# Performance work log

Hardware: AMD Instinct MI355X
Metric: run time of the kernel (lower is better)

The kernel has to match this reference:

```python
import jax, jax.numpy as jnp
import numpy as np

TEMP = 1.0
PRIOR = 0.2
THRESHOLD = 0.5
EPS = 1.1920929e-07  # torch float32 eps used by probs_to_logits / clamp_probs


def setup_inputs() -> dict:
    key = jax.random.key(0)
    k1, k2, k3, k4, k5 = jax.random.split(key, 5)
    B, L, D = 8, 8192, 256
    hidden = jax.random.normal(k1, (B, L, D), dtype=jnp.float32)
    # q/k projections are initialized to identity in the module; perturb slightly
    Wq = jnp.eye(D, dtype=jnp.float32) + 0.02 * jax.random.normal(k2, (D, D), dtype=jnp.float32)
    Wk = jnp.eye(D, dtype=jnp.float32) + 0.02 * jax.random.normal(k3, (D, D), dtype=jnp.float32)
    # uniform noise for the RelaxedBernoulli reparameterized sample
    noise = jax.random.uniform(k4, (B, L), dtype=jnp.float32)
    # ragged lengths -> contiguous attention mask (1s then 0s), as the module assumes
    lengths = jax.random.randint(k5, (B,), L // 2, L + 1)
    attention_mask = (jnp.arange(L)[None, :] < lengths[:, None]).astype(jnp.float32)
    return {"hidden": hidden, "Wq": Wq, "Wk": Wk, "noise": noise, "attention_mask": attention_mask}


def _binomial_loss(k, n, p):
    # -log Binomial(n, p).log_prob(k) / n
    logp = (jax.scipy.special.gammaln(n + 1.0)
            - jax.scipy.special.gammaln(k + 1.0)
            - jax.scipy.special.gammaln(n - k + 1.0)
            + k * jnp.log(p) + (n - k) * jnp.log1p(-p))
    return -logp / n


def reference(hidden, Wq, Wk, noise, attention_mask):
    B, L, D = hidden.shape
    # F.normalize along last dim (eps=1e-12), then linear projections (no bias)
    hn = hidden / jnp.maximum(jnp.linalg.norm(hidden, axis=-1, keepdims=True), 1e-12)
    q = jnp.einsum('bld,ed->ble', hn[:, :-1], Wq)
    k = jnp.einsum('bld,ed->ble', hn[:, 1:], Wk)
    cos_sim = jnp.sum(q * k, axis=-1)                      # [B, L-1]
    probs = jnp.clip((1.0 - cos_sim) * 0.5, 0.0, 1.0)
    probs = jnp.pad(probs, ((0, 0), (1, 0)), constant_values=1.0)  # boundary forced at t=0

    # RelaxedBernoulli(temp, probs).rsample() with externally supplied uniforms
    p = jnp.clip(probs, EPS, 1.0 - EPS)
    logits = jnp.log(p) - jnp.log1p(-p)
    u = jnp.clip(noise, EPS, 1.0 - EPS)
    soft = jax.nn.sigmoid((logits + jnp.log(u) - jnp.log1p(-u)) / TEMP)
    hard = (soft > THRESHOLD).astype(soft.dtype)
    hard = jax.lax.stop_gradient(hard - soft) + soft       # straight-through

    # mask out boundaries in padding; force a boundary at the last real token
    hard = hard * attention_mask
    pad_mask = attention_mask == 0
    first_pad = pad_mask & (jnp.cumsum(pad_mask.astype(jnp.int32), axis=1) == 1)
    last_real = jnp.roll(first_pad, shift=-1, axis=1).at[:, -1].set(False)
    hard = jnp.maximum(hard, last_real.astype(hard.dtype))

    # downsample: mean-pool tokens within each boundary-delimited segment.
    # boundary==1 starts a new segment; segment id = cumsum(hard) - 1.
    hard_bin = jax.lax.stop_gradient(hard) > 0.5
    seg = jnp.cumsum(hard_bin.astype(jnp.int32), axis=1) - 1
    seg = jnp.clip(seg, 0, L - 1)
    flat_seg = (seg + jnp.arange(B, dtype=jnp.int32)[:, None] * L).reshape(-1)  # [B*L]
    w = attention_mask.reshape(-1)                                              # pads excluded
    sums = jax.ops.segment_sum(hidden.reshape(-1, D) * w[:, None], flat_seg, num_segments=B * L)
    cnts = jax.ops.segment_sum(w, flat_seg, num_segments=B * L)
    pooled = (sums / (cnts + 1e-9)[:, None]).reshape(B, L, D)  # [B, S_max<=L, D], zero-padded

    n_b = jnp.sum(hard, axis=1)                  # boundaries per batch row
    num_boundaries = jnp.sum(n_b)
    total_positions = jnp.sum(attention_mask)
    # gathered mask values at kept positions are all 1 -> prefix-ones of length n_b
    shortened_attention_mask = (jnp.arange(L)[None, :]
                                < jax.lax.stop_gradient(n_b)[:, None]).astype(jnp.float32)
    loss = _binomial_loss(num_boundaries, total_positions, PRIOR)
    return pooled, loss, num_boundaries, total_positions, shortened_attention_mask
```

## Files before the change

### kernel.cpp

```cpp
#include <hip/hip_runtime.h>
#include <hip/hip_bf16.h>
#include <math.h>

#define L_SEQ 8192
#define B_BATCH 8
#define D_DIM 256
#define BL (B_BATCH * L_SEQ)
#define EPS_F 1.1920929e-07f

typedef __attribute__((ext_vector_type(8))) short short8;
typedef __attribute__((ext_vector_type(4))) float f32x4;
typedef __attribute__((ext_vector_type(4))) unsigned short u16x4;


__device__ inline unsigned short f2bf(float x) {
    __hip_bfloat16 b = __float2bfloat16(x);
    return *(unsigned short*)&b;
}
__device__ inline float bf2f(unsigned short u) {
    __hip_bfloat16 b = *(__hip_bfloat16*)&u;
    return __bfloat162float(b);
}

__global__ __launch_bounds__(256) void k_matMpack(
    const float* __restrict__ Wq, const float* __restrict__ Wk,
    unsigned short* __restrict__ Bpack) {
    __shared__ float Aq[64][33];
    __shared__ float Ak[64][17];
    const int f   = blockIdx.x;
    const int k8  = f >> 4, ct = f & 15;
    const int tid = threadIdx.x;
    const int n   = tid & 15;
    const int k   = tid >> 4;
    float a0 = 0.f, a1 = 0.f;
    for (int e0 = 0; e0 < 256; e0 += 64) {
        for (int i = tid; i < 64 * 32; i += 256) {
            const int e = i >> 5, d = i & 31;
            Aq[e][d] = Wq[(e0 + e) * 256 + k8 * 32 + d];
        }
        for (int i = tid; i < 64 * 16; i += 256) {
            const int e = i >> 4, d = i & 15;
            Ak[e][d] = Wk[(e0 + e) * 256 + ct * 16 + d];
        }
        __syncthreads();
#pragma unroll 8
        for (int e = 0; e < 64; ++e) {
            a0 += Aq[e][k] * Ak[e][n];
            a1 += Aq[e][k + 16] * Ak[e][n];
        }
        __syncthreads();
    }
    const int col = ct * 16 + n;
    const float M0 = a0 - ((k8 * 32 + k)      == col ? 1.0f : 0.0f);
    const float M1 = a1 - ((k8 * 32 + k + 16) == col ? 1.0f : 0.0f);
    const unsigned short h0 = f2bf(M0), h1 = f2bf(M1);
    const unsigned short l0 = f2bf(M0 - bf2f(h0)), l1 = f2bf(M1 - bf2f(h1));
    unsigned short* dstH = Bpack + (size_t)(k8 * 16 + ct) * 512;
    unsigned short* dstL = dstH + 128 * 512;
    const int q0 = k >> 3, j0 = k & 7;
    const int q1 = (k + 16) >> 3;
    dstH[(q0 * 16 + n) * 8 + j0] = h0;
    dstH[(q1 * 16 + n) * 8 + j0] = h1;
    dstL[(q0 * 16 + n) * 8 + j0] = l0;
    dstL[(q1 * 16 + n) * 8 + j0] = l1;
}

#define RS 264
#define MM(A,Bv,C) __builtin_amdgcn_mfma_f32_16x16x32_bf16((A),(Bv),(C),0,0,0)
#define MFMA8(V0,V1,BN) \
    acc[0][0]=MM(V0,BN##_0,acc[0][0]); acc[0][1]=MM(V0,BN##_1,acc[0][1]); \
    acc[0][2]=MM(V0,BN##_2,acc[0][2]); acc[0][3]=MM(V0,BN##_3,acc[0][3]); \
    acc[1][0]=MM(V1,BN##_0,acc[1][0]); acc[1][1]=MM(V1,BN##_1,acc[1][1]); \
    acc[1][2]=MM(V1,BN##_2,acc[1][2]); acc[1][3]=MM(V1,BN##_3,acc[1][3]);
#define LOADB(BN,S) \
    BN##_0 = Bld[(((S) * 16) + wc4 + 0) * 64]; \
    BN##_1 = Bld[(((S) * 16) + wc4 + 1) * 64]; \
    BN##_2 = Bld[(((S) * 16) + wc4 + 2) * 64]; \
    BN##_3 = Bld[(((S) * 16) + wc4 + 3) * 64];
#define STRIP_HL(S,BN) { \
    const int co = ((S) & 7) * 32; \
    const short8 hv0 = *(const short8*)(hA0 + co), hv1 = *(const short8*)(hA1 + co); \
    const short8 lv0 = *(const short8*)(lA0 + co), lv1 = *(const short8*)(lA1 + co); \
    MFMA8(hv0, hv1, BN); \
    MFMA8(lv0, lv1, BN); \
    LOADB(BN, (S) + 3); }
#define STRIP_H(S,BN) { \
    const int co = ((S) & 7) * 32; \
    const short8 hv0 = *(const short8*)(hA0 + co), hv1 = *(const short8*)(hA1 + co); \
    MFMA8(hv0, hv1, BN); \
    if ((S) + 3 < 16) { LOADB(BN, (S) + 3); } }

__global__ __launch_bounds__(256, 2) void k_cosmfma(
    const float* __restrict__ hidden, const unsigned short* __restrict__ Bpack,
    const float* __restrict__ noise, unsigned char* __restrict__ hard) {
    __shared__ __attribute__((aligned(16))) unsigned short hiA[33 * RS];
    __shared__ __attribute__((aligned(16))) unsigned short loA[33 * RS];
    __shared__ float Vpart[4][32];
    __shared__ float dots[32];

    const int tid  = threadIdx.x;
    const int lane = tid & 63;
    const int w    = tid >> 6;
    const int wc4  = w * 4;
    const int T0   = blockIdx.x * 32;

    const short8* __restrict__ Bld = (const short8*)Bpack + lane;

    short8 bA_0, bA_1, bA_2, bA_3, bB_0, bB_1, bB_2, bB_3, bC_0, bC_1, bC_2, bC_3;
    LOADB(bA, 0);
    LOADB(bB, 1);
    LOADB(bC, 2);

    {
        const int r0 = w * 8;
        int tokA = T0 - 1 + r0; if (tokA < 0) tokA = 0;
        float4 vb0 = ((const float4*)hidden)[(size_t)tokA * 64 + lane];
        float4 vb1 = ((const float4*)hidden)[(size_t)(T0 + r0) * 64 + lane];
        float4 hp4 = {0.f, 0.f, 0.f, 0.f};
#pragma unroll 1
        for (int ii = 0; ii <= 8; ++ii) {
            const float4 vcur = vb0;
            vb0 = vb1;
            if (ii + 2 <= 8)
                vb1 = ((const float4*)hidden)[(size_t)(T0 + r0 + ii + 1) * 64 + lane];
            float ss = vcur.x * vcur.x + vcur.y * vcur.y + vcur.z * vcur.z + vcur.w * vcur.w;
#pragma unroll
            for (int sh = 32; sh >= 1; sh >>= 1) ss += __shfl_xor(ss, sh);
            const float inv = 1.0f / fmaxf(sqrtf(ss), 1e-12f);
            float4 h4;
            h4.x = vcur.x * inv; h4.y = vcur.y * inv;
            h4.z = vcur.z * inv; h4.w = vcur.w * inv;
            const unsigned short hx = f2bf(h4.x), hy = f2bf(h4.y),
                                 hz = f2bf(h4.z), hw2 = f2bf(h4.w);
            const u16x4 hv4 = {hx, hy, hz, hw2};
            const u16x4 lv4 = {f2bf(h4.x - bf2f(hx)), f2bf(h4.y - bf2f(hy)),
                               f2bf(h4.z - bf2f(hz)), f2bf(h4.w - bf2f(hw2))};
            const int i = r0 + ii;
            *(u16x4*)&hiA[i * RS + lane * 4] = hv4;
            *(u16x4*)&loA[i * RS + lane * 4] = lv4;
            if (ii > 0) {
                float pd = h4.x * hp4.x + h4.y * hp4.y + h4.z * hp4.z + h4.w * hp4.w;
#pragma unroll
                for (int sh = 32; sh >= 1; sh >>= 1) pd += __shfl_xor(pd, sh);
                if (lane == 0) dots[i - 1] = pd;
            }
            hp4 = h4;
        }
    }
    __syncthreads();

    const int m = lane & 15, q = lane >> 4;
    const unsigned short* __restrict__ hA0 = &hiA[( 0 + m) * RS + q * 8];
    const unsigned short* __restrict__ hA1 = &hiA[(16 + m) * RS + q * 8];
    const unsigned short* __restrict__ lA0 = &loA[( 0 + m) * RS + q * 8];
    const unsigned short* __restrict__ lA1 = &loA[(16 + m) * RS + q * 8];

    f32x4 acc[2][4];
#pragma unroll
    for (int af = 0; af < 2; ++af)
#pragma unroll
        for (int c = 0; c < 4; ++c) { f32x4 z = {0.f, 0.f, 0.f, 0.f}; acc[af][c] = z; }

    STRIP_HL(0, bA)  STRIP_HL(1, bB)  STRIP_HL(2, bC)  STRIP_HL(3, bA)
    STRIP_HL(4, bB)  STRIP_HL(5, bC)  STRIP_HL(6, bA)  STRIP_HL(7, bB)
    STRIP_H (8, bC)  STRIP_H (9, bA)  STRIP_H (10, bB) STRIP_H (11, bC)
    STRIP_H (12, bA) STRIP_H (13, bB) STRIP_H (14, bC) STRIP_H (15, bA)

#pragma unroll
    for (int af = 0; af < 2; ++af) {
#pragma unroll
        for (int r = 0; r < 4; ++r) {
            const int row = af * 16 + (q << 2) + r;
            const int ib  = (row + 1) * RS + wc4 * 16 + m;
            float pp = acc[af][0][r] * (bf2f(hiA[ib     ]) + bf2f(loA[ib     ]))
                     + acc[af][1][r] * (bf2f(hiA[ib + 16]) + bf2f(loA[ib + 16]))
                     + acc[af][2][r] * (bf2f(hiA[ib + 32]) + bf2f(loA[ib + 32]))
                     + acc[af][3][r] * (bf2f(hiA[ib + 48]) + bf2f(loA[ib + 48]));
            pp += __shfl_xor(pp, 1);
            pp += __shfl_xor(pp, 2);
            pp += __shfl_xor(pp, 4);
            pp += __shfl_xor(pp, 8);
            if (m == 0) Vpart[w][row] = pp;
        }
    }
    __syncthreads();
    if (tid < 32) {
        const int rl = tid;
        const float part = Vpart[0][rl] + Vpart[1][rl] + Vpart[2][rl] + Vpart[3][rl];
        const int t = T0 + rl;
        const int l = t & (L_SEQ - 1);
        float p;
        if (l == 0) {
            p = 1.0f;
        } else {
            p = (1.0f - (part + dots[rl])) * 0.5f;
            p = fminf(fmaxf(p, 0.0f), 1.0f);
        }
        p = fminf(fmaxf(p, EPS_F), 1.0f - EPS_F);
        float u = noise[t];
        u = fminf(fmaxf(u, EPS_F), 1.0f - EPS_F);
        const float z = ((logf(p) - log1pf(-p)) + logf(u)) - log1pf(-u);
        hard[t] = (z > 0.0f) ? (unsigned char)1 : (unsigned char)0;
    }
}

__global__ __launch_bounds__(1024) void k_scan(
    const float* __restrict__ mask, const unsigned char* __restrict__ hard,
    int* __restrict__ starts, int* __restrict__ nb_arr,
    int* __restrict__ len_arr, float* __restrict__ out_short) {
    __shared__ int wsum[16];
    __shared__ int s_len;
    const int b = blockIdx.x, tid = threadIdx.x;
    const int lane = tid & 63, wv = tid >> 6;
    const int base = b * L_SEQ;

    const float4* m4 = (const float4*)(mask + base);
    const float4 va = m4[tid * 2], vb = m4[tid * 2 + 1];
    int cnt = (va.x != 0.f) + (va.y != 0.f) + (va.z != 0.f) + (va.w != 0.f)
            + (vb.x != 0.f) + (vb.y != 0.f) + (vb.z != 0.f) + (vb.w != 0.f);
#pragma unroll
    for (int sh = 32; sh >= 1; sh >>= 1) cnt += __shfl_xor(cnt, sh);
    if (lane == 0) wsum[wv] = cnt;
    __syncthreads();
    if (tid == 0) {
        int s = 0;
        for (int i = 0; i < 16; ++i) s += wsum[i];
        s_len = s;
    }
    __syncthreads();
    const int len = s_len;

    const int i0 = tid * 8;
    const uint2 hb = ((const uint2*)(hard + base))[tid];
    int c = 0;
    unsigned int bits = 0;
#pragma unroll
    for (int j = 0; j < 8; ++j) {
        const unsigned int byte = ((j < 4 ? hb.x : hb.y) >> (8 * (j & 3))) & 0xffu;
        int h = ((i0 + j) < len) ? (int)(byte != 0u) : 0;
        if (len < L_SEQ && (i0 + j) == len - 1) h = 1;
        bits |= (unsigned int)h << j;
        c += h;
    }
    int x = c;
#pragma unroll
    for (int ofs = 1; ofs < 64; ofs <<= 1) {
        const int t = __shfl_up(x, ofs);
        if (lane >= ofs) x += t;
    }
    if (lane == 63) wsum[wv] = x;
    __syncthreads();
    int woff = 0, nb = 0;
#pragma unroll
    for (int i = 0; i < 16; ++i) {
        const int t = wsum[i];
        nb += t;
        if (i < wv) woff += t;
    }
    int run = woff + x - c;
#pragma unroll
    for (int j = 0; j < 8; ++j)
        if ((bits >> j) & 1u) { starts[base + run] = i0 + j; ++run; }

    if (tid == 0) { nb_arr[b] = nb; len_arr[b] = len; }

    float4 o0, o1;
    o0.x = (i0 + 0) < nb ? 1.f : 0.f; o0.y = (i0 + 1) < nb ? 1.f : 0.f;
    o0.z = (i0 + 2) < nb ? 1.f : 0.f; o0.w = (i0 + 3) < nb ? 1.f : 0.f;
    o1.x = (i0 + 4) < nb ? 1.f : 0.f; o1.y = (i0 + 5) < nb ? 1.f : 0.f;
    o1.z = (i0 + 6) < nb ? 1.f : 0.f; o1.w = (i0 + 7) < nb ? 1.f : 0.f;
    float4* os4 = (float4*)(out_short + base);
    os4[tid * 2] = o0;
    os4[tid * 2 + 1] = o1;
}

__global__ __launch_bounds__(256) void k_pool(
    const float* __restrict__ hidden, const int* __restrict__ starts,
    const int* __restrict__ nb_arr, const int* __restrict__ len_arr,
    float* __restrict__ pooled) {
    const int tid  = threadIdx.x;
    const int lane = tid & 63;
    const int wid  = blockIdx.x * 4 + (tid >> 6);
    const int b    = wid >> 13;
    const int s    = wid & (L_SEQ - 1);
    const int nb   = nb_arr[b];

    float4 res = {0.f, 0.f, 0.f, 0.f};
    if (s < nb) {
        const int start = (s == 0) ? 0 : starts[b * L_SEQ + s];
        const int end   = (s + 1 < nb) ? starts[b * L_SEQ + s + 1] : len_arr[b];
        float4 acc = {0.f, 0.f, 0.f, 0.f};
        for (int t = start; t < end; ++t) {
            const float4 v = ((const float4*)hidden)[(b * L_SEQ + t) * 64 + lane];
            acc.x += v.x; acc.y += v.y; acc.z += v.z; acc.w += v.w;
        }
        const float cntf = (float)(end - start);
        res.x = acc.x / cntf; res.y = acc.y / cntf; res.z = acc.z / cntf; res.w = acc.w / cntf;
    }
    ((float4*)pooled)[(size_t)wid * 64 + lane] = res;
}

__global__ void k_final(const int* __restrict__ nb_arr, const int* __restrict__ len_arr,
                        float* __restrict__ out_scal) {
    if (threadIdx.x == 0) {
        int nb = 0, ln = 0;
        for (int b = 0; b < B_BATCH; ++b) { nb += nb_arr[b]; ln += len_arr[b]; }
        const double k = (double)nb, n = (double)ln;
        const double logp = lgamma(n + 1.0) - lgamma(k + 1.0) - lgamma(n - k + 1.0)
                            + k * log(0.2) + (n - k) * log(0.8);
        const double loss = -logp / n;
        out_scal[0] = (float)loss;
        out_scal[1] = (float)nb;
        out_scal[2] = (float)ln;
    }
}

extern "C" void kernel_launch(void* const* d_in, const int* in_sizes, int n_in,
                              void* d_out, int out_size, void* d_ws, size_t ws_size,
                              hipStream_t stream) {
    const float* hidden = (const float*)d_in[0];
    const float* Wq     = (const float*)d_in[1];
    const float* Wk     = (const float*)d_in[2];
    const float* noise  = (const float*)d_in[3];
    const float* mask   = (const float*)d_in[4];
    float* out = (float*)d_out;
    char* ws = (char*)d_ws;

    int*            starts = (int*)(ws);
    unsigned short* Bpack  = (unsigned short*)(ws + 262144);
    unsigned char*  hard   = (unsigned char*)(ws + 524288);
    int*            nb_arr = (int*)(ws + 589824);
    int*            len_arr= (int*)(ws + 589856);

    float* pooled = out;
    float* scal   = out + (size_t)BL * D_DIM;
    float* shortm = scal + 3;

    k_matMpack<<<128, 256, 0, stream>>>(Wq, Wk, Bpack);
    k_cosmfma <<<BL / 32, 256, 0, stream>>>(hidden, Bpack, noise, hard);
    k_scan    <<<B_BATCH, 1024, 0, stream>>>(mask, hard, starts, nb_arr, len_arr, shortm);
    k_pool    <<<BL / 4, 256, 0, stream>>>(hidden, starts, nb_arr, len_arr, pooled);
    k_final   <<<1, 64, 0, stream>>>(nb_arr, len_arr, scal);
}
```

Baseline: 184.4 us.

## Split normalization and bf16 hi/lo packing into separate prenorm kernel

Moves the per-token L2 normalization, bf16 hi/lo split and adjacent-token dot products into a new kernel that writes them to global scratch (aliased onto the output buffer). The MFMA kernel then just copies the packed rows into shared memory, avoiding recomputing the overlap token and shortening its prologue. It also folds the tiny final loss kernel into the pooling kernel to drop a launch. The trade-off is extra global write and read traffic for the packed intermediates.

```diff
diff --git a/kernel.cpp b/kernel.cpp
--- a/kernel.cpp
+++ b/kernel.cpp
@@ -63,6 +63,48 @@
     dstH[(q1 * 16 + n) * 8 + j0] = h1;
     dstL[(q0 * 16 + n) * 8 + j0] = l0;
     dstL[(q1 * 16 + n) * 8 + j0] = l1;
+}
+
+__global__ __launch_bounds__(256) void k_prenorm(
+    const float* __restrict__ hidden, unsigned short* __restrict__ hiG,
+    unsigned short* __restrict__ loG, float* __restrict__ dotsG) {
+    const int tid  = threadIdx.x;
+    const int lane = tid & 63;
+    const int w    = tid >> 6;
+    const int t0   = (blockIdx.x * 4 + w) * 8;
+    int tokA = t0 - 1; if (tokA < 0) tokA = 0;
+    float4 vb0 = ((const float4*)hidden)[(size_t)tokA * 64 + lane];
+    float4 vb1 = ((const float4*)hidden)[(size_t)t0 * 64 + lane];
+    float4 hp4 = {0.f, 0.f, 0.f, 0.f};
+#pragma unroll 1
+    for (int ii = 0; ii <= 8; ++ii) {
+        const float4 vcur = vb0;
+        vb0 = vb1;
+        if (ii + 2 <= 8)
+            vb1 = ((const float4*)hidden)[(size_t)(t0 + ii + 1) * 64 + lane];
+        float ss = vcur.x * vcur.x + vcur.y * vcur.y + vcur.z * vcur.z + vcur.w * vcur.w;
+#pragma unroll
+        for (int sh = 32; sh >= 1; sh >>= 1) ss += __shfl_xor(ss, sh);
+        const float inv = 1.0f / fmaxf(sqrtf(ss), 1e-12f);
+        float4 h4;
+        h4.x = vcur.x * inv; h4.y = vcur.y * inv;
+        h4.z = vcur.z * inv; h4.w = vcur.w * inv;
+        const unsigned short hx = f2bf(h4.x), hy = f2bf(h4.y),
+                             hz = f2bf(h4.z), hw2 = f2bf(h4.w);
+        const u16x4 hv4 = {hx, hy, hz, hw2};
+        const u16x4 lv4 = {f2bf(h4.x - bf2f(hx)), f2bf(h4.y - bf2f(hy)),
+                           f2bf(h4.z - bf2f(hz)), f2bf(h4.w - bf2f(hw2))};
+        if (ii > 0) {
+            const int tok = t0 - 1 + ii;
+            *(u16x4*)&hiG[(size_t)tok * 256 + lane * 4] = hv4;
+            *(u16x4*)&loG[(size_t)tok * 256 + lane * 4] = lv4;
+            float pd = h4.x * hp4.x + h4.y * hp4.y + h4.z * hp4.z + h4.w * hp4.w;
+#pragma unroll
+            for (int sh = 32; sh >= 1; sh >>= 1) pd += __shfl_xor(pd, sh);
+            if (lane == 0) dotsG[tok] = pd;
+        }
+        hp4 = h4;
+    }
 }
 
 #define RS 264
@@ -91,12 +133,12 @@
     if ((S) + 3 < 16) { LOADB(BN, (S) + 3); } }
 
 __global__ __launch_bounds__(256, 2) void k_cosmfma(
-    const float* __restrict__ hidden, const unsigned short* __restrict__ Bpack,
+    const unsigned short* __restrict__ hiG, const unsigned short* __restrict__ loG,
+    const float* __restrict__ dotsG, const unsigned short* __restrict__ Bpack,
     const float* __restrict__ noise, unsigned char* __restrict__ hard) {
     __shared__ __attribute__((aligned(16))) unsigned short hiA[33 * RS];
     __shared__ __attribute__((aligned(16))) unsigned short loA[33 * RS];
     __shared__ float Vpart[4][32];
-    __shared__ float dots[32];
 
     const int tid  = threadIdx.x;
     const int lane = tid & 63;
@@ -113,38 +155,14 @@
 
     {
         const int r0 = w * 8;
-        int tokA = T0 - 1 + r0; if (tokA < 0) tokA = 0;
-        float4 vb0 = ((const float4*)hidden)[(size_t)tokA * 64 + lane];
-        float4 vb1 = ((const float4*)hidden)[(size_t)(T0 + r0) * 64 + lane];
-        float4 hp4 = {0.f, 0.f, 0.f, 0.f};
-#pragma unroll 1
+#pragma unroll
         for (int ii = 0; ii <= 8; ++ii) {
-            const float4 vcur = vb0;
-            vb0 = vb1;
-            if (ii + 2 <= 8)
-                vb1 = ((const float4*)hidden)[(size_t)(T0 + r0 + ii + 1) * 64 + lane];
-            float ss = vcur.x * vcur.x + vcur.y * vcur.y + vcur.z * vcur.z + vcur.w * vcur.w;
-#pragma unroll
-            for (int sh = 32; sh >= 1; sh >>= 1) ss += __shfl_xor(ss, sh);
-            const float inv = 1.0f / fmaxf(sqrtf(ss), 1e-12f);
-            float4 h4;
-            h4.x = vcur.x * inv; h4.y = vcur.y * inv;
-            h4.z = vcur.z * inv; h4.w = vcur.w * inv;
-            const unsigned short hx = f2bf(h4.x), hy = f2bf(h4.y),
-                                 hz = f2bf(h4.z), hw2 = f2bf(h4.w);
-            const u16x4 hv4 = {hx, hy, hz, hw2};
-            const u16x4 lv4 = {f2bf(h4.x - bf2f(hx)), f2bf(h4.y - bf2f(hy)),
-                               f2bf(h4.z - bf2f(hz)), f2bf(h4.w - bf2f(hw2))};
             const int i = r0 + ii;
-            *(u16x4*)&hiA[i * RS + lane * 4] = hv4;
-            *(u16x4*)&loA[i * RS + lane * 4] = lv4;
-            if (ii > 0) {
-                float pd = h4.x * hp4.x + h4.y * hp4.y + h4.z * hp4.z + h4.w * hp4.w;
-#pragma unroll
-                for (int sh = 32; sh >= 1; sh >>= 1) pd += __shfl_xor(pd, sh);
-                if (lane == 0) dots[i - 1] = pd;
-            }
-            hp4 = h4;
+            int tok = T0 - 1 + i; if (tok < 0) tok = 0;
+            const uint2 hv = ((const uint2*)(hiG + (size_t)tok * 256))[lane];
+            const uint2 lv = ((const uint2*)(loG + (size_t)tok * 256))[lane];
+            *(uint2*)&hiA[i * RS + lane * 4] = hv;
+            *(uint2*)&loA[i * RS + lane * 4] = lv;
         }
     }
     __syncthreads();
@@ -193,7 +211,7 @@
         if (l == 0) {
             p = 1.0f;
         } else {
-            p = (1.0f - (part + dots[rl])) * 0.5f;
+            p = (1.0f - (part + dotsG[t])) * 0.5f;
             p = fminf(fmaxf(p, 0.0f), 1.0f);
         }
         p = fminf(fmaxf(p, EPS_F), 1.0f - EPS_F);
@@ -277,13 +295,24 @@
 __global__ __launch_bounds__(256) void k_pool(
     const float* __restrict__ hidden, const int* __restrict__ starts,
     const int* __restrict__ nb_arr, const int* __restrict__ len_arr,
-    float* __restrict__ pooled) {
+    float* __restrict__ pooled, float* __restrict__ out_scal) {
     const int tid  = threadIdx.x;
     const int lane = tid & 63;
     const int wid  = blockIdx.x * 4 + (tid >> 6);
     const int b    = wid >> 13;
     const int s    = wid & (L_SEQ - 1);
     const int nb   = nb_arr[b];
+
+    if (blockIdx.x == 0 && tid == 0) {
+        int nbt = 0, ln = 0;
+        for (int i = 0; i < B_BATCH; ++i) { nbt += nb_arr[i]; ln += len_arr[i]; }
+        const double k = (double)nbt, n = (double)ln;
+        const double logp = lgamma(n + 1.0) - lgamma(k + 1.0) - lgamma(n - k + 1.0)
+                            + k * log(0.2) + (n - k) * log(0.8);
+        out_scal[0] = (float)(-logp / n);
+        out_scal[1] = (float)nbt;
+        out_scal[2] = (float)ln;
+    }
 
     float4 res = {0.f, 0.f, 0.f, 0.f};
     if (s < nb) {
@@ -298,21 +327,6 @@
         res.x = acc.x / cntf; res.y = acc.y / cntf; res.z = acc.z / cntf; res.w = acc.w / cntf;
     }
     ((float4*)pooled)[(size_t)wid * 64 + lane] = res;
-}
-
-__global__ void k_final(const int* __restrict__ nb_arr, const int* __restrict__ len_arr,
-                        float* __restrict__ out_scal) {
-    if (threadIdx.x == 0) {
-        int nb = 0, ln = 0;
-        for (int b = 0; b < B_BATCH; ++b) { nb += nb_arr[b]; ln += len_arr[b]; }
-        const double k = (double)nb, n = (double)ln;
-        const double logp = lgamma(n + 1.0) - lgamma(k + 1.0) - lgamma(n - k + 1.0)
-                            + k * log(0.2) + (n - k) * log(0.8);
-        const double loss = -logp / n;
-        out_scal[0] = (float)loss;
-        out_scal[1] = (float)nb;
-        out_scal[2] = (float)ln;
-    }
 }
 
 extern "C" void kernel_launch(void* const* d_in, const int* in_sizes, int n_in,
@@ -336,9 +350,13 @@
     float* scal   = out + (size_t)BL * D_DIM;
     float* shortm = scal + 3;
 
+    unsigned short* hiG   = (unsigned short*)out;
+    unsigned short* loG   = hiG + (size_t)BL * 256;
+    float*          dotsG = shortm;
+
     k_matMpack<<<128, 256, 0, stream>>>(Wq, Wk, Bpack);
-    k_cosmfma <<<BL / 32, 256, 0, stream>>>(hidden, Bpack, noise, hard);
+    k_prenorm <<<BL / 32, 256, 0, stream>>>(hidden, hiG, loG, dotsG);
+    k_cosmfma <<<BL / 32, 256, 0, stream>>>(hiG, loG, dotsG, Bpack, noise, hard);
     k_scan    <<<B_BATCH, 1024, 0, stream>>>(mask, hard, starts, nb_arr, len_arr, shortm);
-    k_pool    <<<BL / 4, 256, 0, stream>>>(hidden, starts, nb_arr, len_arr, pooled);
-    k_final   <<<1, 64, 0, stream>>>(nb_arr, len_arr, scal);
-}
+    k_pool    <<<BL / 4, 256, 0, stream>>>(hidden, starts, nb_arr, len_arr, pooled, scal);
+}
```

Result: slower. 196.5 us (+6.6%).
